# Optimization experiments

Hardware: AMD Instinct MI355X
Metric: run time of the kernel (lower is better)

The kernel has to match this reference:

```python
import jax, jax.numpy as jnp
import numpy as np

B, D, H, O = 131072, 64, 512, 16

def setup_inputs() -> dict:
    key = jax.random.key(0)
    k1, k2, k3, k4, k5 = jax.random.split(key, 5)
    return {
        "x": jax.random.normal(k1, (B, D), dtype=jnp.float32),
        "centroid": jax.random.uniform(k2, (H, D), dtype=jnp.float32),
        "sigma": jax.random.uniform(k3, (H,), dtype=jnp.float32),
        "weight": jax.random.uniform(k4, (H, O), dtype=jnp.float32),
        "bias": jax.random.uniform(k5, (O,), dtype=jnp.float32),
    }

def reference(x, centroid, sigma, weight, bias):
    # squared euclidean distance between each sample and each centroid: [B, H]
    x_sq = jnp.sum(x * x, axis=1, keepdims=True)            # [B, 1]
    c_sq = jnp.sum(centroid * centroid, axis=1)             # [H]
    sq_dist = x_sq + c_sq[None, :] - 2.0 * (x @ centroid.T)  # [B, H]
    # Gaussian RBF activation per hidden unit
    hidden = jnp.exp(-sq_dist / (2.0 * sigma * sigma))       # [B, H]
    # linear output + bias, then normalize by sum over outputs (per sample)
    out = hidden @ weight + bias                             # [B, O]
    out = out / jnp.sum(out, axis=-1, keepdims=True)
    return out
```

## Files before the change

### kernel.cpp

```cpp
#include <hip/hip_runtime.h>
#include <hip/hip_bf16.h>


#define NDIM 64
#define NHID 512
#define NOUT 16

typedef __attribute__((ext_vector_type(8))) short bf16x8;
typedef __attribute__((ext_vector_type(4))) float f32x4;

#if __has_builtin(__builtin_amdgcn_exp2f)
#define EXP2F(x) __builtin_amdgcn_exp2f(x)
#else
#define EXP2F(x) exp2f(x)
#endif

static __device__ __forceinline__ short f2bf(float f) {
    unsigned int u = __float_as_uint(f);
    unsigned int r = (u + 0x7FFFu + ((u >> 16) & 1u)) >> 16;
    return (short)r;
}

__global__ __launch_bounds__(256, 2)
void rbf_fused(const float* __restrict__ x, const float* __restrict__ cen,
               const float* __restrict__ sig, const float* __restrict__ wgt,
               const float* __restrict__ bias, float* __restrict__ out)
{
    __shared__ __align__(16) short x_lds[16][72];
    __shared__ float xsq_lds[16];
    __shared__ __align__(16) short hid[4][16][136];
    __shared__ __align__(16) float part[4][16][16];

    const int tid   = threadIdx.x;
    const int w     = tid >> 6;
    const int lane  = tid & 63;
    const int g     = lane >> 4;
    const int c     = lane & 15;
    const int hbase = w * 128;

    bf16x8 b1[8][2];
    float A2c[8], AHc[8], NBc[8];
#pragma unroll
    for (int nt = 0; nt < 8; ++nt) {
        const int h = hbase + nt * 16 + c;
        const float* cr = cen + (long)h * NDIM + g * 8;
        float csq = 0.f;
        bf16x8 fr0, fr1;
        {
            f32x4 v0 = *(const f32x4*)(cr);
            f32x4 v1 = *(const f32x4*)(cr + 4);
            csq += v0[0]*v0[0] + v0[1]*v0[1] + v0[2]*v0[2] + v0[3]*v0[3];
            csq += v1[0]*v1[0] + v1[1]*v1[1] + v1[2]*v1[2] + v1[3]*v1[3];
            fr0[0]=f2bf(v0[0]); fr0[1]=f2bf(v0[1]); fr0[2]=f2bf(v0[2]); fr0[3]=f2bf(v0[3]);
            fr0[4]=f2bf(v1[0]); fr0[5]=f2bf(v1[1]); fr0[6]=f2bf(v1[2]); fr0[7]=f2bf(v1[3]);
        }
        {
            f32x4 v0 = *(const f32x4*)(cr + 32);
            f32x4 v1 = *(const f32x4*)(cr + 36);
            csq += v0[0]*v0[0] + v0[1]*v0[1] + v0[2]*v0[2] + v0[3]*v0[3];
            csq += v1[0]*v1[0] + v1[1]*v1[1] + v1[2]*v1[2] + v1[3]*v1[3];
            fr1[0]=f2bf(v0[0]); fr1[1]=f2bf(v0[1]); fr1[2]=f2bf(v0[2]); fr1[3]=f2bf(v0[3]);
            fr1[4]=f2bf(v1[0]); fr1[5]=f2bf(v1[1]); fr1[6]=f2bf(v1[2]); fr1[7]=f2bf(v1[3]);
        }
        b1[nt][0] = fr0; b1[nt][1] = fr1;
        csq += __shfl_xor(csq, 16);
        csq += __shfl_xor(csq, 32);
        float s = sig[h];
        float a = 1.4426950408889634f / (2.0f * s * s);
        a = fminf(a, 1e30f);
        A2c[nt] = 2.0f * a;
        AHc[nt] = a;
        NBc[nt] = -a * csq;
    }

    bf16x8 w2[4];
#pragma unroll
    for (int ks = 0; ks < 4; ++ks) {
        bf16x8 f;
#pragma unroll
        for (int j = 0; j < 8; ++j) {
            f[j] = f2bf(wgt[(hbase + ks * 32 + g * 8 + j) * NOUT + c]);
        }
        w2[ks] = f;
    }
    const float biasv = bias[c];

    const long rowblock = (long)blockIdx.x * 128;

    for (int ms = 0; ms < 8; ++ms) {
        __syncthreads();
        {
            const int r = tid >> 4, cc = tid & 15;
            const float* xp = x + (rowblock + ms * 16 + r) * NDIM + cc * 4;
            f32x4 v = *(const f32x4*)xp;
            float sq = v[0]*v[0] + v[1]*v[1] + v[2]*v[2] + v[3]*v[3];
            sq += __shfl_xor(sq, 1);
            sq += __shfl_xor(sq, 2);
            sq += __shfl_xor(sq, 4);
            sq += __shfl_xor(sq, 8);
            short4 s4;
            s4.x = f2bf(v[0]); s4.y = f2bf(v[1]); s4.z = f2bf(v[2]); s4.w = f2bf(v[3]);
            *(short4*)&x_lds[r][cc * 4] = s4;
            if (cc == 0) xsq_lds[r] = sq;
        }
        __syncthreads();

        bf16x8 af0 = *(const bf16x8*)&x_lds[c][g * 8];
        bf16x8 af1 = *(const bf16x8*)&x_lds[c][32 + g * 8];
        f32x4 xs4 = *(const f32x4*)&xsq_lds[4 * g];

#pragma unroll
        for (int nt = 0; nt < 8; ++nt) {
            f32x4 acc = {0.f, 0.f, 0.f, 0.f};
            acc = __builtin_amdgcn_mfma_f32_16x16x32_bf16(af0, b1[nt][0], acc, 0, 0, 0);
            acc = __builtin_amdgcn_mfma_f32_16x16x32_bf16(af1, b1[nt][1], acc, 0, 0, 0);
#pragma unroll
            for (int r = 0; r < 4; ++r) {
                float nbx = fmaf(-AHc[nt], xs4[r], NBc[nt]);
                float arg = fmaf(A2c[nt], acc[r], nbx);
                hid[w][4 * g + r][nt * 16 + c] = f2bf(EXP2F(arg));
            }
        }

        f32x4 acc2 = {0.f, 0.f, 0.f, 0.f};
#pragma unroll
        for (int ks = 0; ks < 4; ++ks) {
            bf16x8 a2 = *(const bf16x8*)&hid[w][c][ks * 32 + g * 8];
            acc2 = __builtin_amdgcn_mfma_f32_16x16x32_bf16(a2, w2[ks], acc2, 0, 0, 0);
        }
        *(f32x4*)&part[w][c][4 * g] = acc2;
        __syncthreads();

        {
            const int m = tid >> 4, o = tid & 15;
            float v = biasv + part[0][o][m] + part[1][o][m] + part[2][o][m] + part[3][o][m];
            float s = v;
            s += __shfl_xor(s, 1);
            s += __shfl_xor(s, 2);
            s += __shfl_xor(s, 4);
            s += __shfl_xor(s, 8);
            out[(rowblock + ms * 16 + m) * NOUT + o] = v / s;
        }
    }
}

extern "C" void kernel_launch(void* const* d_in, const int* in_sizes, int n_in,
                              void* d_out, int out_size, void* d_ws, size_t ws_size,
                              hipStream_t stream) {
    const float* x    = (const float*)d_in[0];
    const float* cen  = (const float*)d_in[1];
    const float* sig  = (const float*)d_in[2];
    const float* wgt  = (const float*)d_in[3];
    const float* bias = (const float*)d_in[4];
    float* out = (float*)d_out;
    (void)in_sizes; (void)n_in; (void)d_ws; (void)ws_size; (void)out_size;

    rbf_fused<<<dim3(1024), dim3(256), 0, stream>>>(x, cen, sig, wgt, bias, out);
}
```

Baseline: 121.4 us.

## Double-buffer x tile with register prefetch, swizzle hidden LDS, raise occupancy

Each x row tile is now loaded into registers one iteration ahead and written into a second LDS buffer after the current tile's MMAs. This removes one barrier per iteration and hides global load latency behind compute. The hidden-activation LDS tile drops its padding in favour of an XOR swizzle, and the partial-sum array gets a new pad, both to cut bank conflicts. Launch bounds now ask for 4 blocks per CU, which may force register spilling given the large per-thread centroid fragment arrays.

```diff
diff --git a/kernel.cpp b/kernel.cpp
--- a/kernel.cpp
+++ b/kernel.cpp
@@ -21,21 +21,21 @@
     return (short)r;
 }
 
-__global__ __launch_bounds__(256, 2)
+__global__ __launch_bounds__(256, 4)
 void rbf_fused(const float* __restrict__ x, const float* __restrict__ cen,
                const float* __restrict__ sig, const float* __restrict__ wgt,
                const float* __restrict__ bias, float* __restrict__ out)
 {
-    __shared__ __align__(16) short x_lds[16][72];
-    __shared__ float xsq_lds[16];
-    __shared__ __align__(16) short hid[4][16][136];
-    __shared__ __align__(16) float part[4][16][16];
+    __shared__ __align__(16) short x_lds[2][16][72];
+    __shared__ __align__(16) float xsq_lds[2][16];
+    __shared__ __align__(16) short hid[4][16 * 128];
+    __shared__ __align__(16) float part[4][16][20];
 
-    const int tid   = threadIdx.x;
-    const int w     = tid >> 6;
-    const int lane  = tid & 63;
-    const int g     = lane >> 4;
-    const int c     = lane & 15;
+    const int tid  = threadIdx.x;
+    const int w    = tid >> 6;
+    const int lane = tid & 63;
+    const int g    = lane >> 4;
+    const int c    = lane & 15;
     const int hbase = w * 128;
 
     bf16x8 b1[8][2];
@@ -86,28 +86,36 @@
     const float biasv = bias[c];
 
     const long rowblock = (long)blockIdx.x * 128;
+    const int r  = tid >> 4;
+    const int cc = tid & 15;
+    const float* xp = x + (rowblock + r) * NDIM + cc * 4;
+    float* outp = out + rowblock * NOUT;
+    short* hid_w = hid[w];
+
+    {
+        f32x4 v = *(const f32x4*)xp;
+        float sq = v[0]*v[0] + v[1]*v[1] + v[2]*v[2] + v[3]*v[3];
+        sq += __shfl_xor(sq, 1);
+        sq += __shfl_xor(sq, 2);
+        sq += __shfl_xor(sq, 4);
+        sq += __shfl_xor(sq, 8);
+        short4 s4;
+        s4.x = f2bf(v[0]); s4.y = f2bf(v[1]); s4.z = f2bf(v[2]); s4.w = f2bf(v[3]);
+        *(short4*)&x_lds[0][r][cc * 4] = s4;
+        if (cc == 0) xsq_lds[0][r] = sq;
+    }
 
     for (int ms = 0; ms < 8; ++ms) {
-        __syncthreads();
-        {
-            const int r = tid >> 4, cc = tid & 15;
-            const float* xp = x + (rowblock + ms * 16 + r) * NDIM + cc * 4;
-            f32x4 v = *(const f32x4*)xp;
-            float sq = v[0]*v[0] + v[1]*v[1] + v[2]*v[2] + v[3]*v[3];
-            sq += __shfl_xor(sq, 1);
-            sq += __shfl_xor(sq, 2);
-            sq += __shfl_xor(sq, 4);
-            sq += __shfl_xor(sq, 8);
-            short4 s4;
-            s4.x = f2bf(v[0]); s4.y = f2bf(v[1]); s4.z = f2bf(v[2]); s4.w = f2bf(v[3]);
-            *(short4*)&x_lds[r][cc * 4] = s4;
-            if (cc == 0) xsq_lds[r] = sq;
-        }
+        const int cur = ms & 1;
+
+        f32x4 vnext;
+        if (ms < 7) vnext = *(const f32x4*)(xp + (ms + 1) * 16 * NDIM);
+
         __syncthreads();
 
-        bf16x8 af0 = *(const bf16x8*)&x_lds[c][g * 8];
-        bf16x8 af1 = *(const bf16x8*)&x_lds[c][32 + g * 8];
-        f32x4 xs4 = *(const f32x4*)&xsq_lds[4 * g];
+        bf16x8 af0 = *(const bf16x8*)&x_lds[cur][c][g * 8];
+        bf16x8 af1 = *(const bf16x8*)&x_lds[cur][c][32 + g * 8];
+        f32x4 xs4 = *(const f32x4*)&xsq_lds[cur][4 * g];
 
 #pragma unroll
         for (int nt = 0; nt < 8; ++nt) {
@@ -115,31 +123,50 @@
             acc = __builtin_amdgcn_mfma_f32_16x16x32_bf16(af0, b1[nt][0], acc, 0, 0, 0);
             acc = __builtin_amdgcn_mfma_f32_16x16x32_bf16(af1, b1[nt][1], acc, 0, 0, 0);
 #pragma unroll
-            for (int r = 0; r < 4; ++r) {
-                float nbx = fmaf(-AHc[nt], xs4[r], NBc[nt]);
-                float arg = fmaf(A2c[nt], acc[r], nbx);
-                hid[w][4 * g + r][nt * 16 + c] = f2bf(EXP2F(arg));
+            for (int rr = 0; rr < 4; ++rr) {
+                float nbx = fmaf(-AHc[nt], xs4[rr], NBc[nt]);
+                float arg = fmaf(A2c[nt], acc[rr], nbx);
+                int byte = ((4 * g + rr) << 8) + ((nt * 16 + c) << 1);
+                byte ^= (g << 5);
+                hid_w[byte >> 1] = f2bf(EXP2F(arg));
             }
         }
 
         f32x4 acc2 = {0.f, 0.f, 0.f, 0.f};
 #pragma unroll
         for (int ks = 0; ks < 4; ++ks) {
-            bf16x8 a2 = *(const bf16x8*)&hid[w][c][ks * 32 + g * 8];
+            int byte = (c << 8) + ((ks * 32 + g * 8) << 1);
+            byte ^= ((c >> 2) << 5);
+            bf16x8 a2 = *(const bf16x8*)&hid_w[byte >> 1];
             acc2 = __builtin_amdgcn_mfma_f32_16x16x32_bf16(a2, w2[ks], acc2, 0, 0, 0);
         }
         *(f32x4*)&part[w][c][4 * g] = acc2;
+
+        if (ms < 7) {
+            float sq = vnext[0]*vnext[0] + vnext[1]*vnext[1]
+                     + vnext[2]*vnext[2] + vnext[3]*vnext[3];
+            sq += __shfl_xor(sq, 1);
+            sq += __shfl_xor(sq, 2);
+            sq += __shfl_xor(sq, 4);
+            sq += __shfl_xor(sq, 8);
+            short4 s4;
+            s4.x = f2bf(vnext[0]); s4.y = f2bf(vnext[1]);
+            s4.z = f2bf(vnext[2]); s4.w = f2bf(vnext[3]);
+            *(short4*)&x_lds[cur ^ 1][r][cc * 4] = s4;
+            if (cc == 0) xsq_lds[cur ^ 1][r] = sq;
+        }
+
         __syncthreads();
 
         {
-            const int m = tid >> 4, o = tid & 15;
-            float v = biasv + part[0][o][m] + part[1][o][m] + part[2][o][m] + part[3][o][m];
+            float v = biasv + part[0][cc][r] + part[1][cc][r]
+                            + part[2][cc][r] + part[3][cc][r];
             float s = v;
             s += __shfl_xor(s, 1);
             s += __shfl_xor(s, 2);
             s += __shfl_xor(s, 4);
             s += __shfl_xor(s, 8);
-            out[(rowblock + ms * 16 + m) * NOUT + o] = v / s;
+            outp[ms * 16 * NOUT + r * NOUT + cc] = v / s;
         }
     }
 }
```

After: 244.2 us. +101.1%, slower.

## Split work by rows per wave, precompute centroid and weight fragments in a prep kernel

Applied to the files above, without the earlier changes.

A small prep kernel converts the centroids and weights to bf16 MFMA fragment layout and precomputes the per-hidden-unit exp coefficients into workspace. The main kernel now gives each wave its own 32 rows and loops over all 512 hidden units, streaming centroid and weight fragments from global/L2. This removes the cross-wave partial-sum reduction and most block-wide barriers, using a double-buffered per-wave LDS tile for the hidden activations. In exchange it adds a second launch and reloads the fragments from cache for every wave instead of keeping them in registers.

```diff
diff --git a/kernel.cpp b/kernel.cpp
--- a/kernel.cpp
+++ b/kernel.cpp
@@ -5,9 +5,11 @@
 #define NDIM 64
 #define NHID 512
 #define NOUT 16
+#define LOG2E 1.4426950408889634f
 
 typedef __attribute__((ext_vector_type(8))) short bf16x8;
 typedef __attribute__((ext_vector_type(4))) float f32x4;
+typedef __attribute__((ext_vector_type(2))) float f32x2;
 
 #if __has_builtin(__builtin_amdgcn_exp2f)
 #define EXP2F(x) __builtin_amdgcn_exp2f(x)
@@ -21,126 +23,133 @@
     return (short)r;
 }
 
+#define WS_CFRAG 0
+#define WS_WFRAG 65536
+#define WS_COF   81920
+
+__global__ __launch_bounds__(64)
+void rbf_prep(const float* __restrict__ cen, const float* __restrict__ sig,
+              const float* __restrict__ wgt, char* __restrict__ ws)
+{
+    const int blk = blockIdx.x;
+    const int d = threadIdx.x;
+    if (blk < NHID) {
+        const int h = blk;
+        const float v = cen[h * NDIM + d];
+        float sq = v * v;
+        sq += __shfl_xor(sq, 1);
+        sq += __shfl_xor(sq, 2);
+        sq += __shfl_xor(sq, 4);
+        sq += __shfl_xor(sq, 8);
+        sq += __shfl_xor(sq, 16);
+        sq += __shfl_xor(sq, 32);
+        if (d == 0) {
+            float s = sig[h];
+            float a = LOG2E / (2.0f * s * s);
+            a = fminf(a, 1e30f);
+            f32x2 cf; cf[0] = a; cf[1] = -a * sq;
+            *(f32x2*)(ws + WS_COF + h * 8) = cf;
+        }
+        const int nt = h >> 4, cp = h & 15, kc = d >> 5, g = (d >> 3) & 3, j = d & 7;
+        const int byte = (((nt * 2 + kc) * 64) + g * 16 + cp) * 16 + j * 2;
+        *(short*)(ws + WS_CFRAG + byte) = f2bf(v);
+    } else {
+        const int ks = blk - NHID;
+        const int g = d >> 4, c = d & 15;
+        bf16x8 f;
+#pragma unroll
+        for (int j = 0; j < 8; ++j)
+            f[j] = f2bf(wgt[(ks * 32 + g * 8 + j) * NOUT + c]);
+        *(bf16x8*)(ws + WS_WFRAG + (ks * 64 + d) * 16) = f;
+    }
+}
+
 __global__ __launch_bounds__(256, 2)
-void rbf_fused(const float* __restrict__ x, const float* __restrict__ cen,
-               const float* __restrict__ sig, const float* __restrict__ wgt,
-               const float* __restrict__ bias, float* __restrict__ out)
+void rbf_main(const float* __restrict__ x, const float* __restrict__ bias,
+              const char* __restrict__ ws, float* __restrict__ out)
 {
-    __shared__ __align__(16) short x_lds[16][72];
-    __shared__ float xsq_lds[16];
-    __shared__ __align__(16) short hid[4][16][136];
-    __shared__ __align__(16) float part[4][16][16];
+    __shared__ __align__(16) short hidb[4][2][32][40];
 
-    const int tid   = threadIdx.x;
-    const int w     = tid >> 6;
-    const int lane  = tid & 63;
-    const int g     = lane >> 4;
-    const int c     = lane & 15;
-    const int hbase = w * 128;
+    const int tid  = threadIdx.x;
+    const int w    = tid >> 6;
+    const int lane = tid & 63;
+    const int g    = lane >> 4;
+    const int c    = lane & 15;
+    const long r0  = (long)blockIdx.x * 128 + w * 32;
 
-    bf16x8 b1[8][2];
-    float A2c[8], AHc[8], NBc[8];
+    const bf16x8* cfrag = (const bf16x8*)(ws + WS_CFRAG);
+    const bf16x8* wfrag = (const bf16x8*)(ws + WS_WFRAG);
+    const char*   cofp  = ws + WS_COF;
+
+    bf16x8 A[2][2];
+    float xs4[2][4];
 #pragma unroll
-    for (int nt = 0; nt < 8; ++nt) {
-        const int h = hbase + nt * 16 + c;
-        const float* cr = cen + (long)h * NDIM + g * 8;
-        float csq = 0.f;
-        bf16x8 fr0, fr1;
-        {
-            f32x4 v0 = *(const f32x4*)(cr);
-            f32x4 v1 = *(const f32x4*)(cr + 4);
-            csq += v0[0]*v0[0] + v0[1]*v0[1] + v0[2]*v0[2] + v0[3]*v0[3];
-            csq += v1[0]*v1[0] + v1[1]*v1[1] + v1[2]*v1[2] + v1[3]*v1[3];
-            fr0[0]=f2bf(v0[0]); fr0[1]=f2bf(v0[1]); fr0[2]=f2bf(v0[2]); fr0[3]=f2bf(v0[3]);
-            fr0[4]=f2bf(v1[0]); fr0[5]=f2bf(v1[1]); fr0[6]=f2bf(v1[2]); fr0[7]=f2bf(v1[3]);
+    for (int mg = 0; mg < 2; ++mg) {
+        const float* xr = x + (r0 + mg * 16 + c) * NDIM;
+        float sqs = 0.f;
+#pragma unroll
+        for (int kc = 0; kc < 2; ++kc) {
+            f32x4 v0 = *(const f32x4*)(xr + kc * 32 + g * 8);
+            f32x4 v1 = *(const f32x4*)(xr + kc * 32 + g * 8 + 4);
+            sqs += v0[0]*v0[0] + v0[1]*v0[1] + v0[2]*v0[2] + v0[3]*v0[3];
+            sqs += v1[0]*v1[0] + v1[1]*v1[1] + v1[2]*v1[2] + v1[3]*v1[3];
+            bf16x8 f;
+            f[0]=f2bf(v0[0]); f[1]=f2bf(v0[1]); f[2]=f2bf(v0[2]); f[3]=f2bf(v0[3]);
+            f[4]=f2bf(v1[0]); f[5]=f2bf(v1[1]); f[6]=f2bf(v1[2]); f[7]=f2bf(v1[3]);
+            A[mg][kc] = f;
         }
-        {
-            f32x4 v0 = *(const f32x4*)(cr + 32);
-            f32x4 v1 = *(const f32x4*)(cr + 36);
-            csq += v0[0]*v0[0] + v0[1]*v0[1] + v0[2]*v0[2] + v0[3]*v0[3];
-            csq += v1[0]*v1[0] + v1[1]*v1[1] + v1[2]*v1[2] + v1[3]*v1[3];
-            fr1[0]=f2bf(v0[0]); fr1[1]=f2bf(v0[1]); fr1[2]=f2bf(v0[2]); fr1[3]=f2bf(v0[3]);
-            fr1[4]=f2bf(v1[0]); fr1[5]=f2bf(v1[1]); fr1[6]=f2bf(v1[2]); fr1[7]=f2bf(v1[3]);
-        }
-        b1[nt][0] = fr0; b1[nt][1] = fr1;
-        csq += __shfl_xor(csq, 16);
-        csq += __shfl_xor(csq, 32);
-        float s = sig[h];
-        float a = 1.4426950408889634f / (2.0f * s * s);
-        a = fminf(a, 1e30f);
-        A2c[nt] = 2.0f * a;
-        AHc[nt] = a;
-        NBc[nt] = -a * csq;
+        sqs += __shfl_xor(sqs, 16);
+        sqs += __shfl_xor(sqs, 32);
+#pragma unroll
+        for (int rr = 0; rr < 4; ++rr)
+            xs4[mg][rr] = __shfl(sqs, 4 * g + rr);
     }
 
-    bf16x8 w2[4];
+    f32x4 acc2[2] = {{0.f,0.f,0.f,0.f},{0.f,0.f,0.f,0.f}};
 #pragma unroll
-    for (int ks = 0; ks < 4; ++ks) {
-        bf16x8 f;
+    for (int ks = 0; ks < 16; ++ks) {
 #pragma unroll
-        for (int j = 0; j < 8; ++j) {
-            f[j] = f2bf(wgt[(hbase + ks * 32 + g * 8 + j) * NOUT + c]);
-        }
-        w2[ks] = f;
-    }
-    const float biasv = bias[c];
-
-    const long rowblock = (long)blockIdx.x * 128;
-
-    for (int ms = 0; ms < 8; ++ms) {
-        __syncthreads();
-        {
-            const int r = tid >> 4, cc = tid & 15;
-            const float* xp = x + (rowblock + ms * 16 + r) * NDIM + cc * 4;
-            f32x4 v = *(const f32x4*)xp;
-            float sq = v[0]*v[0] + v[1]*v[1] + v[2]*v[2] + v[3]*v[3];
-            sq += __shfl_xor(sq, 1);
-            sq += __shfl_xor(sq, 2);
-            sq += __shfl_xor(sq, 4);
-            sq += __shfl_xor(sq, 8);
-            short4 s4;
-            s4.x = f2bf(v[0]); s4.y = f2bf(v[1]); s4.z = f2bf(v[2]); s4.w = f2bf(v[3]);
-            *(short4*)&x_lds[r][cc * 4] = s4;
-            if (cc == 0) xsq_lds[r] = sq;
-        }
-        __syncthreads();
-
-        bf16x8 af0 = *(const bf16x8*)&x_lds[c][g * 8];
-        bf16x8 af1 = *(const bf16x8*)&x_lds[c][32 + g * 8];
-        f32x4 xs4 = *(const f32x4*)&xsq_lds[4 * g];
-
+        for (int t = 0; t < 2; ++t) {
+            const int nt = 2 * ks + t;
+            const f32x2 cf = *(const f32x2*)(cofp + (nt * 16 + c) * 8);
+            const float a = cf[0], nb = cf[1];
+            const float A2 = a + a;
+            const bf16x8 b0 = cfrag[(nt * 2 + 0) * 64 + lane];
+            const bf16x8 b1 = cfrag[(nt * 2 + 1) * 64 + lane];
 #pragma unroll
-        for (int nt = 0; nt < 8; ++nt) {
-            f32x4 acc = {0.f, 0.f, 0.f, 0.f};
-            acc = __builtin_amdgcn_mfma_f32_16x16x32_bf16(af0, b1[nt][0], acc, 0, 0, 0);
-            acc = __builtin_amdgcn_mfma_f32_16x16x32_bf16(af1, b1[nt][1], acc, 0, 0, 0);
+            for (int mg = 0; mg < 2; ++mg) {
+                f32x4 z = {0.f, 0.f, 0.f, 0.f};
+                f32x4 acc = __builtin_amdgcn_mfma_f32_16x16x32_bf16(A[mg][0], b0, z, 0, 0, 0);
+                acc = __builtin_amdgcn_mfma_f32_16x16x32_bf16(A[mg][1], b1, acc, 0, 0, 0);
 #pragma unroll
-            for (int r = 0; r < 4; ++r) {
-                float nbx = fmaf(-AHc[nt], xs4[r], NBc[nt]);
-                float arg = fmaf(A2c[nt], acc[r], nbx);
-                hid[w][4 * g + r][nt * 16 + c] = f2bf(EXP2F(arg));
+                for (int rr = 0; rr < 4; ++rr) {
+                    float nbx = fmaf(-a, xs4[mg][rr], nb);
+                    float arg = fmaf(A2, acc[rr], nbx);
+                    hidb[w][ks & 1][mg * 16 + 4 * g + rr][t * 16 + c] = f2bf(EXP2F(arg));
+                }
             }
         }
+        const bf16x8 wf  = wfrag[ks * 64 + lane];
+        const bf16x8 a20 = *(const bf16x8*)&hidb[w][ks & 1][c][g * 8];
+        const bf16x8 a21 = *(const bf16x8*)&hidb[w][ks & 1][c + 16][g * 8];
+        acc2[0] = __builtin_amdgcn_mfma_f32_16x16x32_bf16(a20, wf, acc2[0], 0, 0, 0);
+        acc2[1] = __builtin_amdgcn_mfma_f32_16x16x32_bf16(a21, wf, acc2[1], 0, 0, 0);
+    }
 
-        f32x4 acc2 = {0.f, 0.f, 0.f, 0.f};
+    const float bv = bias[c];
 #pragma unroll
-        for (int ks = 0; ks < 4; ++ks) {
-            bf16x8 a2 = *(const bf16x8*)&hid[w][c][ks * 32 + g * 8];
-            acc2 = __builtin_amdgcn_mfma_f32_16x16x32_bf16(a2, w2[ks], acc2, 0, 0, 0);
+    for (int mg = 0; mg < 2; ++mg) {
+        f32x4 v, s;
+#pragma unroll
+        for (int rr = 0; rr < 4; ++rr) { v[rr] = acc2[mg][rr] + bv; s[rr] = v[rr]; }
+#pragma unroll
+        for (int off = 1; off <= 8; off <<= 1) {
+#pragma unroll
+            for (int rr = 0; rr < 4; ++rr) s[rr] += __shfl_xor(s[rr], off);
         }
-        *(f32x4*)&part[w][c][4 * g] = acc2;
-        __syncthreads();
-
-        {
-            const int m = tid >> 4, o = tid & 15;
-            float v = biasv + part[0][o][m] + part[1][o][m] + part[2][o][m] + part[3][o][m];
-            float s = v;
-            s += __shfl_xor(s, 1);
-            s += __shfl_xor(s, 2);
-            s += __shfl_xor(s, 4);
-            s += __shfl_xor(s, 8);
-            out[(rowblock + ms * 16 + m) * NOUT + o] = v / s;
-        }
+#pragma unroll
+        for (int rr = 0; rr < 4; ++rr)
+            out[(r0 + mg * 16 + 4 * g + rr) * NOUT + c] = v[rr] / s[rr];
     }
 }
 
@@ -153,7 +162,9 @@
     const float* wgt  = (const float*)d_in[3];
     const float* bias = (const float*)d_in[4];
     float* out = (float*)d_out;
-    (void)in_sizes; (void)n_in; (void)d_ws; (void)ws_size; (void)out_size;
+    (void)in_sizes; (void)n_in; (void)ws_size; (void)out_size;
 
-    rbf_fused<<<dim3(1024), dim3(256), 0, stream>>>(x, cen, sig, wgt, bias, out);
+    char* ws = (char*)d_ws;
+    rbf_prep<<<dim3(NHID + 16), dim3(64), 0, stream>>>(cen, sig, wgt, ws);
+    rbf_main<<<dim3(1024), dim3(256), 0, stream>>>(x, bias, ws, out);
 }
```

Measured after the change: 102.6 us. 1.18x faster.
